# Optimization experiments

Hardware: AMD Instinct MI355X
Metric: run time of the kernel (lower is better)

The kernel has to match this reference:

```python
import jax, jax.numpy as jnp
import numpy as np

NEG_SLOPE = 0.2  # PyG GATv2Conv default negative_slope
EPS = 1e-16      # PyG softmax denominator eps


def _gatv2_conv(x, src, dst, Wl, bl, Wr, br, att, bias, heads, out_ch):
    """PyG GATv2Conv (share_weights=False, concat=True, self-loops already in edges)."""
    N = x.shape[0]
    xl = (x @ Wl + bl).reshape(N, heads, out_ch)  # values / source transform
    xr = (x @ Wr + br).reshape(N, heads, out_ch)  # target transform
    m = jax.nn.leaky_relu(xl[src] + xr[dst], NEG_SLOPE)      # [E,H,C]
    e = jnp.einsum('ehc,hc->eh', m, att)                      # [E,H]
    emax = jax.ops.segment_max(e, dst, num_segments=N)       # [N,H]
    ee = jnp.exp(e - emax[dst])
    denom = jax.ops.segment_sum(ee, dst, num_segments=N)
    alpha = ee / (denom[dst] + EPS)                           # scatter-softmax over dst
    out = jax.ops.segment_sum(xl[src] * alpha[:, :, None], dst, num_segments=N)
    return out.reshape(N, heads * out_ch) + bias


def setup_inputs() -> dict:
    key = jax.random.key(0)
    ks = jax.random.split(key, 16)
    N, E, DIN, DH, H, DOUT = 50000, 800000, 128, 16, 8, 64
    x = jax.random.normal(ks[0], (N, DIN), dtype=jnp.float32)
    edge_index = jax.random.randint(ks[1], (2, E), 0, N, dtype=jnp.int64)
    g = lambda k, shape: jax.random.normal(k, shape, dtype=jnp.float32) * (1.0 / np.sqrt(shape[0]))
    params = {
        'Wl1': g(ks[2], (DIN, H * DH)), 'bl1': jnp.zeros((H * DH,), jnp.float32),
        'Wr1': g(ks[3], (DIN, H * DH)), 'br1': jnp.zeros((H * DH,), jnp.float32),
        'att1': g(ks[4], (H, DH)), 'bias1': jnp.zeros((H * DH,), jnp.float32),
        'Wl2': g(ks[5], (H * DH, DOUT)), 'bl2': jnp.zeros((DOUT,), jnp.float32),
        'Wr2': g(ks[6], (H * DH, DOUT)), 'br2': jnp.zeros((DOUT,), jnp.float32),
        'att2': g(ks[7], (1, DOUT)), 'bias2': jnp.zeros((DOUT,), jnp.float32),
    }
    return {'x': x, 'edge_index': edge_index, **params}


def reference(x, edge_index, Wl1, bl1, Wr1, br1, att1, bias1,
              Wl2, bl2, Wr2, br2, att2, bias2):
    N = x.shape[0]
    loop = jnp.arange(N, dtype=edge_index.dtype)
    ei = jnp.concatenate([edge_index, jnp.stack([loop, loop])], axis=1)  # add self-loops
    src, dst = ei[0], ei[1]
    # eval mode: F.dropout is identity (p=0.6 dropouts skipped)
    h = _gatv2_conv(x, src, dst, Wl1, bl1, Wr1, br1, att1, bias1, heads=8, out_ch=16)
    h = jax.nn.elu(h)
    h = _gatv2_conv(h, src, dst, Wl2, bl2, Wr2, br2, att2, bias2, heads=1, out_ch=64)
    out = jax.nn.log_softmax(h, axis=1)
    predictions = jnp.argmax(out, axis=1)
    return (h, out, predictions)
```

## Files before the change

### kernel.cpp

```cpp
#include <hip/hip_runtime.h>
#include <hip/hip_bf16.h>

typedef unsigned short u16;
typedef __attribute__((ext_vector_type(8))) short bf8v;
typedef __attribute__((ext_vector_type(4))) float f4v;

#define N_NODES 50000
#define N_EDGES 800000
#define ET (N_EDGES + N_NODES)
#define D1 128
#define D2 64
#define NEG 0.2f
#define EPSF 1e-16f
#define NTILES_PAD 3128
#define NP (NTILES_PAD * 16)

#define O_XL1    0
#define O_XR1    6400000
#define O_AH     12800000
#define O_AM     16003072
#define O_AL     19206144
#define O_B1H    22409216
#define O_B1M    22425600
#define O_B1L    22441984
#define O_B2H    22458368
#define O_B2M    22466560
#define O_B2L    22474752
#define O_WF     22482944
#define O_SRC    22483968
#define O_DST    22908968
#define O_DEG    23333968
#define O_ROWPTR 23383968
#define O_RANK   23433969
#define O_CSR    23858969
#define O_FLAGS  24283969
#define O_PART   24283971

#define W_BL1   0
#define W_BR1   128
#define W_ATT1  256
#define W_BIAS1 384
#define W_BL2   512
#define W_BR2   576
#define W_ATT2  640
#define W_BIAS2 704

#define NB_SCAN  196
#define NB_CVT   3321
#define NB_PACKX 3128
#define NB_PK    (NB_SCAN + NB_PACKX + 128 + 64 + 1)
#define NB_G1    3128
#define NB_SG    (NB_G1 + NB_CVT)

__device__ __forceinline__ float load_f32(const void* src, int i, int isbf16) {
    if (isbf16) {
        u16 u = ((const u16*)src)[i];
        return __uint_as_float((unsigned)u << 16);
    }
    return ((const float*)src)[i];
}
__device__ __forceinline__ u16 f2b(float v) {
    __hip_bfloat16 h = __float2bfloat16(v);
    return *(u16*)&h;
}
__device__ __forceinline__ float b2f(u16 u) { return __uint_as_float((unsigned)u << 16); }

__device__ __forceinline__ void split3(float v, u16& hi, u16& mid, u16& lo) {
    hi = f2b(v);
    float r1 = v - b2f(hi);
    mid = f2b(r1);
    float r2 = r1 - b2f(mid);
    lo = f2b(r2);
}

__global__ void init_k(int* deg, const u16* x16, const int* ei32, int* flags) {
    int b = blockIdx.x;
    if (b < NB_SCAN) {
        int i = b * 256 + threadIdx.x;
        if (i < N_NODES) deg[i] = 0;
        return;
    }
    int lane = threadIdx.x;
    if (lane >= 64) return;
    int hits = 0;
    for (int j = lane; j < 32768; j += 64) {
        u16 u = x16[2 * j];
        if (((u >> 7) & 0xFF) == 0xFF) hits++;
    }
#pragma unroll
    for (int off = 32; off > 0; off >>= 1) hits += __shfl_xor(hits, off);
    int nz = 0;
    if (lane < 32) nz = ei32[2 * lane + 1];
#pragma unroll
    for (int off = 32; off > 0; off >>= 1) nz |= __shfl_xor(nz, off);
    if (lane == 0) { flags[0] = hits ? 0 : 1; flags[1] = nz ? 0 : 1; }
}

__global__ void cvt_k(const int* __restrict__ ei, const int* __restrict__ flags,
                      u16* __restrict__ srcA, u16* __restrict__ dstA,
                      u16* __restrict__ rank, int* __restrict__ deg) {
    int e = blockIdx.x * 256 + threadIdx.x;
    if (e >= ET) return;
    int s, d;
    if (e < N_EDGES) {
        if (flags[1]) { s = ei[2 * e]; d = ei[2 * (N_EDGES + e)]; }
        else          { s = ei[e];     d = ei[N_EDGES + e]; }
    } else {
        s = d = e - N_EDGES;
    }
    srcA[e] = (u16)s; dstA[e] = (u16)d;
    rank[e] = (u16)atomicAdd(&deg[d], 1);
}

__global__ void pk_k(const int* __restrict__ deg, int* __restrict__ part,
                     const void* x, u16* AH, u16* AM, u16* AL,
                     const void* Wl1, const void* Wr1, u16* B1H, u16* B1M, u16* B1L,
                     const void* Wl2, const void* Wr2, u16* B2H, u16* B2M, u16* B2L,
                     const void* bl1, const void* br1, const void* att1, const void* bias1,
                     const void* bl2, const void* br2, const void* att2, const void* bias2,
                     float* Wf, const int* flags) {
    int b = blockIdx.x, t = threadIdx.x;
    int fb = flags[0];
    if (b < NB_SCAN) {
        __shared__ int s[256];
        int i = b * 256 + t;
        s[t] = (i < N_NODES) ? deg[i] : 0;
        __syncthreads();
        for (int off = 128; off > 0; off >>= 1) {
            if (t < off) s[t] += s[t + off];
            __syncthreads();
        }
        if (t == 0) part[b] = s[0];
        return;
    }
    b -= NB_SCAN;
    if (b < NB_PACKX) {
        int i = b * 256 + t;
        int j = i * 8;
        int tile = j >> 11;
        int jj = j & 2047;
        int r = tile * 16 + ((jj >> 3) & 15);
        int k0 = (jj >> 7) * 8;
        uint4 H = {0, 0, 0, 0}, M = {0, 0, 0, 0}, L = {0, 0, 0, 0};
        u16* Hp = (u16*)&H; u16* Mp = (u16*)&M; u16* Lp = (u16*)&L;
        if (r < N_NODES) {
            if (fb) {
                H = *(const uint4*)((const u16*)x + r * D1 + k0);
            } else {
                float4 xa = *(const float4*)((const float*)x + r * D1 + k0);
                float4 xb = *(const float4*)((const float*)x + r * D1 + k0 + 4);
                float vv[8] = {xa.x, xa.y, xa.z, xa.w, xb.x, xb.y, xb.z, xb.w};
#pragma unroll
                for (int e2 = 0; e2 < 8; e2++) split3(vv[e2], Hp[e2], Mp[e2], Lp[e2]);
            }
        }
        *(uint4*)(AH + j) = H;
        *(uint4*)(AM + j) = M;
        *(uint4*)(AL + j) = L;
        return;
    }
    b -= NB_PACKX;
    if (b < 128) {
        int i = b * 256 + t;
        int k = i >> 8, n = i & 255;
        float v = (n < 128) ? load_f32(Wl1, k * 128 + n, fb)
                            : load_f32(Wr1, k * 128 + (n - 128), fb);
        u16 hi, mid, lo; split3(v, hi, mid, lo);
        int idx = ((k >> 3) * 256 + n) * 8 + (k & 7);
        B1H[idx] = hi; B1M[idx] = mid; B1L[idx] = lo;
        return;
    }
    b -= 128;
    if (b < 64) {
        int i = b * 256 + t;
        int k = i >> 7, n = i & 127;
        float v = (n < 64) ? load_f32(Wl2, k * 64 + n, fb)
                           : load_f32(Wr2, k * 64 + (n - 64), fb);
        u16 hi, mid, lo; split3(v, hi, mid, lo);
        int idx = ((k >> 3) * 128 + n) * 8 + (k & 7);
        B2H[idx] = hi; B2M[idx] = mid; B2L[idx] = lo;
        return;
    }
    if (t < 128) {
        Wf[W_BL1 + t]   = load_f32(bl1, t, fb);
        Wf[W_BR1 + t]   = load_f32(br1, t, fb);
        Wf[W_ATT1 + t]  = load_f32(att1, t, fb);
        Wf[W_BIAS1 + t] = load_f32(bias1, t, fb);
        if (t < 64) {
            Wf[W_BL2 + t]   = load_f32(bl2, t, fb);
            Wf[W_BR2 + t]   = load_f32(br2, t, fb);
            Wf[W_ATT2 + t]  = load_f32(att2, t, fb);
            Wf[W_BIAS2 + t] = load_f32(bias2, t, fb);
        }
    }
}

__global__ __launch_bounds__(256) void scanB_k(int* __restrict__ part) {
    __shared__ int s[256];
    int t = threadIdx.x;
    s[t] = (t < NB_SCAN) ? part[t] : 0;
    __syncthreads();
    for (int off = 1; off < 256; off <<= 1) {
        int v = (t >= off) ? s[t - off] : 0;
        __syncthreads();
        s[t] += v;
        __syncthreads();
    }
    if (t < NB_SCAN) part[t] = (t == 0) ? 0 : s[t - 1];
}

__global__ __launch_bounds__(256) void scanC_k(const int* __restrict__ deg, const int* __restrict__ part,
                                               int* __restrict__ rowptr) {
    __shared__ int s[256];
    int t = threadIdx.x, i = blockIdx.x * 256 + t;
    int v = (i < N_NODES) ? deg[i] : 0;
    s[t] = v;
    __syncthreads();
    for (int off = 1; off < 256; off <<= 1) {
        int u = (t >= off) ? s[t - off] : 0;
        __syncthreads();
        s[t] += u;
        __syncthreads();
    }
    int excl = part[blockIdx.x] + s[t] - v;
    if (i < N_NODES) rowptr[i] = excl;
    if (i == N_NODES - 1) rowptr[N_NODES] = excl + v;
}

#define MFMA6(acc, ah, am, al, bh, bm, bl)                                    \
    acc = __builtin_amdgcn_mfma_f32_16x16x32_bf16(ah, bl, acc, 0, 0, 0);      \
    acc = __builtin_amdgcn_mfma_f32_16x16x32_bf16(am, bm, acc, 0, 0, 0);      \
    acc = __builtin_amdgcn_mfma_f32_16x16x32_bf16(al, bh, acc, 0, 0, 0);      \
    acc = __builtin_amdgcn_mfma_f32_16x16x32_bf16(ah, bm, acc, 0, 0, 0);      \
    acc = __builtin_amdgcn_mfma_f32_16x16x32_bf16(am, bh, acc, 0, 0, 0);      \
    acc = __builtin_amdgcn_mfma_f32_16x16x32_bf16(ah, bh, acc, 0, 0, 0);

__global__ __launch_bounds__(256) void sg_k(const u16* __restrict__ AH, const u16* __restrict__ AM,
                                            const u16* __restrict__ AL,
                                            const u16* __restrict__ BH, const u16* __restrict__ BM,
                                            const u16* __restrict__ BL,
                                            const float* __restrict__ Wf,
                                            float* __restrict__ xl, float* __restrict__ xr,
                                            const u16* __restrict__ srcA, const u16* __restrict__ dstA,
                                            const u16* __restrict__ rank, const int* __restrict__ rowptr,
                                            u16* __restrict__ csr) {
    int b = blockIdx.x;
    if (b < NB_G1) {
        int w = threadIdx.x >> 6, l = threadIdx.x & 63;
        int tile = (b >> 2) * 4 + w;
        int cb = (b & 3) << 6;
        int lr = l & 15, lg = l >> 4;
        f4v acc[4];
#pragma unroll
        for (int nt = 0; nt < 4; nt++) acc[nt] = (f4v)(0.f);
        int aoff = tile * 2048 + lg * 128 + lr * 8;
#pragma unroll
        for (int ks = 0; ks < 4; ks++) {
            bf8v ah = *(const bf8v*)(AH + aoff + ks * 512);
            bf8v am = *(const bf8v*)(AM + aoff + ks * 512);
            bf8v al = *(const bf8v*)(AL + aoff + ks * 512);
            int boff = ((ks * 4 + lg) * 256 + cb + lr) * 8;
#pragma unroll
            for (int nt = 0; nt < 4; nt++) {
                bf8v bh = *(const bf8v*)(BH + boff + nt * 128);
                bf8v bm = *(const bf8v*)(BM + boff + nt * 128);
                bf8v bl = *(const bf8v*)(BL + boff + nt * 128);
                MFMA6(acc[nt], ah, am, al, bh, bm, bl)
            }
        }
        int r0 = tile * 16 + lg * 4;
        if (r0 >= N_NODES) return;
#pragma unroll
        for (int nt = 0; nt < 4; nt++) {
            int col = cb + nt * 16 + lr;
            float bias = (col < D1) ? Wf[W_BL1 + col] : Wf[W_BR1 + col - D1];
            float* dst = (col < D1) ? (xl + col) : (xr + col - D1);
#pragma unroll
            for (int j = 0; j < 4; j++) {
                int row = r0 + j;
                dst[(size_t)row * D1] = acc[nt][j] + bias;
            }
        }
        return;
    }
    int e = (b - NB_G1) * 256 + threadIdx.x;
    if (e < ET) {
        int d = dstA[e];
        csr[rowptr[d] + rank[e]] = srcA[e];
    }
}

__global__ __launch_bounds__(256) void gemm2_mfma(const u16* __restrict__ AH, const u16* __restrict__ AM,
                                                  const u16* __restrict__ AL,
                                                  const u16* __restrict__ BH, const u16* __restrict__ BM,
                                                  const u16* __restrict__ BL,
                                                  const float* __restrict__ Wf,
                                                  float* __restrict__ xl2, float* __restrict__ xr2) {
    int w = threadIdx.x >> 6, l = threadIdx.x & 63;
    int tile = blockIdx.x * 4 + w;
    int cb = blockIdx.y << 6;
    int lr = l & 15, lg = l >> 4;
    f4v acc[4];
#pragma unroll
    for (int nt = 0; nt < 4; nt++) acc[nt] = (f4v)(0.f);
    int aoff = tile * 2048 + lg * 128 + lr * 8;
#pragma unroll
    for (int ks = 0; ks < 4; ks++) {
        bf8v ah = *(const bf8v*)(AH + aoff + ks * 512);
        bf8v am = *(const bf8v*)(AM + aoff + ks * 512);
        bf8v al = *(const bf8v*)(AL + aoff + ks * 512);
        int boff = ((ks * 4 + lg) * 128 + cb + lr) * 8;
#pragma unroll
        for (int nt = 0; nt < 4; nt++) {
            bf8v bh = *(const bf8v*)(BH + boff + nt * 128);
            bf8v bm = *(const bf8v*)(BM + boff + nt * 128);
            bf8v bl = *(const bf8v*)(BL + boff + nt * 128);
            MFMA6(acc[nt], ah, am, al, bh, bm, bl)
        }
    }
    int r0 = tile * 16 + lg * 4;
    if (r0 >= N_NODES) return;
#pragma unroll
    for (int nt = 0; nt < 4; nt++) {
        int col = cb + nt * 16 + lr;
        float bias = (col < D2) ? Wf[W_BL2 + col] : Wf[W_BR2 + col - D2];
        float* dst = (col < D2) ? (xl2 + col) : (xr2 + col - D2);
#pragma unroll
        for (int j = 0; j < 4; j++) {
            int row = r0 + j;
            dst[(size_t)row * D2] = acc[nt][j] + bias;
        }
    }
}

#define L1STEP(a)                                                              \
    {                                                                          \
        float m0 = a.x + xr4.x; m0 = fmaxf(m0, NEG * m0);                      \
        float m1 = a.y + xr4.y; m1 = fmaxf(m1, NEG * m1);                      \
        float m2 = a.z + xr4.z; m2 = fmaxf(m2, NEG * m2);                      \
        float m3 = a.w + xr4.w; m3 = fmaxf(m3, NEG * m3);                      \
        float p = m0 * at4.x + m1 * at4.y + m2 * at4.z + m3 * at4.w;           \
        p += __shfl_xor(p, 1);                                                 \
        p += __shfl_xor(p, 2);                                                 \
        p = fminf(fmaxf(p, -60.f), 60.f);                                      \
        float wgt = __expf(p);                                                 \
        l += wgt;                                                              \
        acc.x = fmaf(wgt, a.x, acc.x);                                         \
        acc.y = fmaf(wgt, a.y, acc.y);                                         \
        acc.z = fmaf(wgt, a.z, acc.z);                                         \
        acc.w = fmaf(wgt, a.w, acc.w);                                         \
    }

__global__ __launch_bounds__(256) void l1_agg(const int* __restrict__ rowptr, const u16* __restrict__ csr,
                                              const float* __restrict__ xl, const float* __restrict__ xr,
                                              const float* __restrict__ Wf,
                                              u16* __restrict__ A2H, u16* __restrict__ A2M, u16* __restrict__ A2L) {
    int n = (blockIdx.x * 256 + threadIdx.x) >> 5;
    int q = threadIdx.x & 31;
    const float4* xl4 = (const float4*)xl;
    float4 xr4 = ((const float4*)(xr + (size_t)n * D1))[q];
    float4 at4 = ((const float4*)(Wf + W_ATT1))[q];
    int i0 = rowptr[n], i1 = rowptr[n + 1];
    float l = 0.f;
    float4 acc = {0.f, 0.f, 0.f, 0.f};
    float4 a = xl4[(size_t)csr[i0] * 32 + q];
    for (int i = i0 + 1; i < i1; i++) {
        float4 an = xl4[(size_t)csr[i] * 32 + q];
        L1STEP(a)
        a = an;
    }
    L1STEP(a)
    float rinv = 1.f / l;
    float4 bi4 = ((const float4*)(Wf + W_BIAS1))[q];
    float v0 = acc.x * rinv + bi4.x; v0 = v0 > 0.f ? v0 : expm1f(v0);
    float v1 = acc.y * rinv + bi4.y; v1 = v1 > 0.f ? v1 : expm1f(v1);
    float v2 = acc.z * rinv + bi4.z; v2 = v2 > 0.f ? v2 : expm1f(v2);
    float v3 = acc.w * rinv + bi4.w; v3 = v3 > 0.f ? v3 : expm1f(v3);
    int base = (n >> 4) * 2048 + (q >> 1) * 128 + (n & 15) * 8 + (q & 1) * 4;
    ushort4 h4, m4, l4;
    split3(v0, h4.x, m4.x, l4.x);
    split3(v1, h4.y, m4.y, l4.y);
    split3(v2, h4.z, m4.z, l4.z);
    split3(v3, h4.w, m4.w, l4.w);
    *(ushort4*)(A2H + base) = h4;
    *(ushort4*)(A2M + base) = m4;
    *(ushort4*)(A2L + base) = l4;
}

#define L2STEP(a)                                                              \
    {                                                                          \
        float m0 = a.x + xr4.x; m0 = fmaxf(m0, NEG * m0);                      \
        float m1 = a.y + xr4.y; m1 = fmaxf(m1, NEG * m1);                      \
        float m2 = a.z + xr4.z; m2 = fmaxf(m2, NEG * m2);                      \
        float m3 = a.w + xr4.w; m3 = fmaxf(m3, NEG * m3);                      \
        float p = m0 * at4.x + m1 * at4.y + m2 * at4.z + m3 * at4.w;           \
        p += __shfl_xor(p, 1);                                                 \
        p += __shfl_xor(p, 2);                                                 \
        p += __shfl_xor(p, 4);                                                 \
        p += __shfl_xor(p, 8);                                                 \
        p = fminf(fmaxf(p, -80.f), 80.f);                                      \
        float wgt = __expf(p);                                                 \
        l += wgt;                                                              \
        acc.x = fmaf(wgt, a.x, acc.x);                                         \
        acc.y = fmaf(wgt, a.y, acc.y);                                         \
        acc.z = fmaf(wgt, a.z, acc.z);                                         \
        acc.w = fmaf(wgt, a.w, acc.w);                                         \
    }

__global__ __launch_bounds__(256) void l2_agg(const int* __restrict__ rowptr, const u16* __restrict__ csr,
                                              const float* __restrict__ xl, const float* __restrict__ xr,
                                              const float* __restrict__ Wf, float* __restrict__ out) {
    int n = (blockIdx.x * 256 + threadIdx.x) >> 4;
    int q = threadIdx.x & 15;
    const float4* xl4 = (const float4*)xl;
    float4 xr4 = ((const float4*)(xr + (size_t)n * D2))[q];
    float4 at4 = ((const float4*)(Wf + W_ATT2))[q];
    int i0 = rowptr[n], i1 = rowptr[n + 1];
    float l = 0.f;
    float4 acc = {0.f, 0.f, 0.f, 0.f};
    float4 a = xl4[(size_t)csr[i0] * 16 + q];
    for (int i = i0 + 1; i < i1; i++) {
        float4 an = xl4[(size_t)csr[i] * 16 + q];
        L2STEP(a)
        a = an;
    }
    L2STEP(a)
    float rinv = 1.f / (l + EPSF);
    float4 bi4 = ((const float4*)(Wf + W_BIAS2))[q];
    float v0 = acc.x * rinv + bi4.x;
    float v1 = acc.y * rinv + bi4.y;
    float v2 = acc.z * rinv + bi4.z;
    float v3 = acc.w * rinv + bi4.w;
    float4 hv = {v0, v1, v2, v3};
    ((float4*)(out + (size_t)n * D2))[q] = hv;
    float mx = fmaxf(fmaxf(v0, v1), fmaxf(v2, v3));
#pragma unroll
    for (int off = 1; off < 16; off <<= 1) mx = fmaxf(mx, __shfl_xor(mx, off));
    float sum = expf(v0 - mx) + expf(v1 - mx) + expf(v2 - mx) + expf(v3 - mx);
#pragma unroll
    for (int off = 1; off < 16; off <<= 1) sum += __shfl_xor(sum, off);
    float lse = mx + logf(sum);
    float4 ls = {v0 - lse, v1 - lse, v2 - lse, v3 - lse};
    ((float4*)(out + (size_t)N_NODES * D2 + (size_t)n * D2))[q] = ls;
    float bv = v0; int bi = 4 * q;
    if (v1 > bv) { bv = v1; bi = 4 * q + 1; }
    if (v2 > bv) { bv = v2; bi = 4 * q + 2; }
    if (v3 > bv) { bv = v3; bi = 4 * q + 3; }
#pragma unroll
    for (int off = 1; off < 16; off <<= 1) {
        float ov = __shfl_xor(bv, off);
        int   oi = __shfl_xor(bi, off);
        if (ov > bv || (ov == bv && oi < bi)) { bv = ov; bi = oi; }
    }
    if (q == 0) out[(size_t)2 * N_NODES * D2 + n] = (float)bi;
}

extern "C" void kernel_launch(void* const* d_in, const int* in_sizes, int n_in,
                              void* d_out, int out_size, void* d_ws, size_t ws_size,
                              hipStream_t stream) {
    const void* x  = d_in[0];
    const int*  ei = (const int*)d_in[1];

    float* ws = (float*)d_ws;
    float* xl1    = ws + O_XL1;
    float* xr1    = ws + O_XR1;
    u16*   AH     = (u16*)(ws + O_AH);
    u16*   AM     = (u16*)(ws + O_AM);
    u16*   AL     = (u16*)(ws + O_AL);
    u16*   B1H    = (u16*)(ws + O_B1H);
    u16*   B1M    = (u16*)(ws + O_B1M);
    u16*   B1L    = (u16*)(ws + O_B1L);
    u16*   B2H    = (u16*)(ws + O_B2H);
    u16*   B2M    = (u16*)(ws + O_B2M);
    u16*   B2L    = (u16*)(ws + O_B2L);
    float* Wf     = ws + O_WF;
    u16*   srcA   = (u16*)(ws + O_SRC);
    u16*   dstA   = (u16*)(ws + O_DST);
    int*   deg    = (int*)(ws + O_DEG);
    int*   rowptr = (int*)(ws + O_ROWPTR);
    u16*   rank   = (u16*)(ws + O_RANK);
    u16*   csr    = (u16*)(ws + O_CSR);
    int*   flags  = (int*)(ws + O_FLAGS);
    int*   part   = (int*)(ws + O_PART);

    float* xl2 = xl1;
    float* xr2 = xl1 + 3200000;

    init_k<<<NB_SCAN + 1, 256, 0, stream>>>(deg, (const u16*)x, ei, flags);
    cvt_k<<<NB_CVT, 256, 0, stream>>>(ei, flags, srcA, dstA, rank, deg);
    pk_k<<<NB_PK, 256, 0, stream>>>(deg, part,
                                    x, AH, AM, AL,
                                    d_in[2], d_in[4], B1H, B1M, B1L,
                                    d_in[8], d_in[10], B2H, B2M, B2L,
                                    d_in[3], d_in[5], d_in[6], d_in[7],
                                    d_in[9], d_in[11], d_in[12], d_in[13],
                                    Wf, flags);
    scanB_k<<<1, 256, 0, stream>>>(part);
    scanC_k<<<NB_SCAN, 256, 0, stream>>>(deg, part, rowptr);
    sg_k<<<NB_SG, 256, 0, stream>>>(AH, AM, AL, B1H, B1M, B1L, Wf, xl1, xr1,
                                    srcA, dstA, rank, rowptr, csr);

    l1_agg<<<6250, 256, 0, stream>>>(rowptr, csr, xl1, xr1, Wf, AH, AM, AL);
    gemm2_mfma<<<dim3(NTILES_PAD / 4, 2), 256, 0, stream>>>(AH, AM, AL, B2H, B2M, B2L, Wf, xl2, xr2);
    l2_agg<<<3125, 256, 0, stream>>>(rowptr, csr, xl2, xr2, Wf, (float*)d_out);
}
```

Before: 254.9 us.

## Degree-sort nodes for aggregation load balance and fuse prep kernels

Builds a degree histogram and counting-sort permutation of nodes, so each aggregation warp group in layer 1 and layer 2 handles nodes of similar degree and divergence within a wave is reduced. The edge-convert kernel is merged into the packing kernel, which removes one launch. Layer-1 output is now written as plain fp32 and split into three bf16 parts inside gemm2, replacing the tiled hi/mid/lo writes. The cost is three extra small scan/histogram passes, atomics on the bucket cursors, and redundant split work in gemm2 because each of its two column blocks reads the same rows.

```diff
diff --git a/kernel.cpp b/kernel.cpp
--- a/kernel.cpp
+++ b/kernel.cpp
@@ -35,6 +35,9 @@
 #define O_CSR    23858969
 #define O_FLAGS  24283969
 #define O_PART   24283971
+#define O_HIST   24284167
+#define O_BCUR   24284423
+#define O_PERM   24284679
 
 #define W_BL1   0
 #define W_BR1   128
@@ -48,7 +51,7 @@
 #define NB_SCAN  196
 #define NB_CVT   3321
 #define NB_PACKX 3128
-#define NB_PK    (NB_SCAN + NB_PACKX + 128 + 64 + 1)
+#define NB_PREP  (NB_CVT + NB_PACKX + 128 + 64 + 1)
 #define NB_G1    3128
 #define NB_SG    (NB_G1 + NB_CVT)
 
@@ -73,11 +76,15 @@
     lo = f2b(r2);
 }
 
-__global__ void init_k(int* deg, const u16* x16, const int* ei32, int* flags) {
+__global__ void init_k(int* deg, const u16* x16, const int* ei32, int* flags, int* hist) {
     int b = blockIdx.x;
     if (b < NB_SCAN) {
         int i = b * 256 + threadIdx.x;
         if (i < N_NODES) deg[i] = 0;
+        return;
+    }
+    if (b == NB_SCAN + 1) {
+        hist[threadIdx.x] = 0;
         return;
     }
     int lane = threadIdx.x;
@@ -96,44 +103,33 @@
     if (lane == 0) { flags[0] = hits ? 0 : 1; flags[1] = nz ? 0 : 1; }
 }
 
-__global__ void cvt_k(const int* __restrict__ ei, const int* __restrict__ flags,
-                      u16* __restrict__ srcA, u16* __restrict__ dstA,
-                      u16* __restrict__ rank, int* __restrict__ deg) {
-    int e = blockIdx.x * 256 + threadIdx.x;
-    if (e >= ET) return;
-    int s, d;
-    if (e < N_EDGES) {
-        if (flags[1]) { s = ei[2 * e]; d = ei[2 * (N_EDGES + e)]; }
-        else          { s = ei[e];     d = ei[N_EDGES + e]; }
-    } else {
-        s = d = e - N_EDGES;
-    }
-    srcA[e] = (u16)s; dstA[e] = (u16)d;
-    rank[e] = (u16)atomicAdd(&deg[d], 1);
-}
-
-__global__ void pk_k(const int* __restrict__ deg, int* __restrict__ part,
-                     const void* x, u16* AH, u16* AM, u16* AL,
-                     const void* Wl1, const void* Wr1, u16* B1H, u16* B1M, u16* B1L,
-                     const void* Wl2, const void* Wr2, u16* B2H, u16* B2M, u16* B2L,
-                     const void* bl1, const void* br1, const void* att1, const void* bias1,
-                     const void* bl2, const void* br2, const void* att2, const void* bias2,
-                     float* Wf, const int* flags) {
+__global__ void prep_k(const int* __restrict__ ei,
+                       u16* __restrict__ srcA, u16* __restrict__ dstA,
+                       u16* __restrict__ rank, int* __restrict__ deg,
+                       const void* x, u16* AH, u16* AM, u16* AL,
+                       const void* Wl1, const void* Wr1, u16* B1H, u16* B1M, u16* B1L,
+                       const void* Wl2, const void* Wr2, u16* B2H, u16* B2M, u16* B2L,
+                       const void* bl1, const void* br1, const void* att1, const void* bias1,
+                       const void* bl2, const void* br2, const void* att2, const void* bias2,
+                       float* Wf, const int* flags) {
     int b = blockIdx.x, t = threadIdx.x;
     int fb = flags[0];
-    if (b < NB_SCAN) {
-        __shared__ int s[256];
-        int i = b * 256 + t;
-        s[t] = (i < N_NODES) ? deg[i] : 0;
-        __syncthreads();
-        for (int off = 128; off > 0; off >>= 1) {
-            if (t < off) s[t] += s[t + off];
-            __syncthreads();
-        }
-        if (t == 0) part[b] = s[0];
-        return;
-    }
-    b -= NB_SCAN;
+    if (b < NB_CVT) {
+        int e = b * 256 + t;
+        if (e < ET) {
+            int s, d;
+            if (e < N_EDGES) {
+                if (flags[1]) { s = ei[2 * e]; d = ei[2 * (N_EDGES + e)]; }
+                else          { s = ei[e];     d = ei[N_EDGES + e]; }
+            } else {
+                s = d = e - N_EDGES;
+            }
+            srcA[e] = (u16)s; dstA[e] = (u16)d;
+            rank[e] = (u16)atomicAdd(&deg[d], 1);
+        }
+        return;
+    }
+    b -= NB_CVT;
     if (b < NB_PACKX) {
         int i = b * 256 + t;
         int j = i * 8;
@@ -195,10 +191,43 @@
     }
 }
 
-__global__ __launch_bounds__(256) void scanB_k(int* __restrict__ part) {
+__global__ __launch_bounds__(256) void sa_k(const int* __restrict__ deg, int* __restrict__ part,
+                                            int* __restrict__ hist) {
+    int b = blockIdx.x, t = threadIdx.x;
+    if (b < NB_SCAN) {
+        __shared__ int s[256];
+        int i = b * 256 + t;
+        s[t] = (i < N_NODES) ? deg[i] : 0;
+        __syncthreads();
+        for (int off = 128; off > 0; off >>= 1) {
+            if (t < off) s[t] += s[t + off];
+            __syncthreads();
+        }
+        if (t == 0) part[b] = s[0];
+        return;
+    }
+    int i = (b - NB_SCAN) * 256 + t;
+    if (i < N_NODES) atomicAdd(&hist[min(deg[i], 255)], 1);
+}
+
+__global__ __launch_bounds__(256) void sb_k(int* __restrict__ part, const int* __restrict__ hist,
+                                            int* __restrict__ bcur) {
     __shared__ int s[256];
     int t = threadIdx.x;
-    s[t] = (t < NB_SCAN) ? part[t] : 0;
+    if (blockIdx.x == 0) {
+        s[t] = (t < NB_SCAN) ? part[t] : 0;
+        __syncthreads();
+        for (int off = 1; off < 256; off <<= 1) {
+            int v = (t >= off) ? s[t - off] : 0;
+            __syncthreads();
+            s[t] += v;
+            __syncthreads();
+        }
+        if (t < NB_SCAN) part[t] = (t == 0) ? 0 : s[t - 1];
+        return;
+    }
+    int h = hist[t];
+    s[t] = h;
     __syncthreads();
     for (int off = 1; off < 256; off <<= 1) {
         int v = (t >= off) ? s[t - off] : 0;
@@ -206,25 +235,35 @@
         s[t] += v;
         __syncthreads();
     }
-    if (t < NB_SCAN) part[t] = (t == 0) ? 0 : s[t - 1];
-}
-
-__global__ __launch_bounds__(256) void scanC_k(const int* __restrict__ deg, const int* __restrict__ part,
-                                               int* __restrict__ rowptr) {
-    __shared__ int s[256];
-    int t = threadIdx.x, i = blockIdx.x * 256 + t;
-    int v = (i < N_NODES) ? deg[i] : 0;
-    s[t] = v;
-    __syncthreads();
-    for (int off = 1; off < 256; off <<= 1) {
-        int u = (t >= off) ? s[t - off] : 0;
+    bcur[t] = s[t] - h;
+}
+
+__global__ __launch_bounds__(256) void sc_k(const int* __restrict__ deg, const int* __restrict__ part,
+                                            int* __restrict__ rowptr,
+                                            int* __restrict__ bcur, int* __restrict__ perm) {
+    int b = blockIdx.x, t = threadIdx.x;
+    if (b < NB_SCAN) {
+        __shared__ int s[256];
+        int i = b * 256 + t;
+        int v = (i < N_NODES) ? deg[i] : 0;
+        s[t] = v;
         __syncthreads();
-        s[t] += u;
-        __syncthreads();
-    }
-    int excl = part[blockIdx.x] + s[t] - v;
-    if (i < N_NODES) rowptr[i] = excl;
-    if (i == N_NODES - 1) rowptr[N_NODES] = excl + v;
+        for (int off = 1; off < 256; off <<= 1) {
+            int u = (t >= off) ? s[t - off] : 0;
+            __syncthreads();
+            s[t] += u;
+            __syncthreads();
+        }
+        int excl = part[b] + s[t] - v;
+        if (i < N_NODES) rowptr[i] = excl;
+        if (i == N_NODES - 1) rowptr[N_NODES] = excl + v;
+        return;
+    }
+    int i = (b - NB_SCAN) * 256 + t;
+    if (i < N_NODES) {
+        int bk = min(deg[i], 255);
+        perm[atomicAdd(&bcur[bk], 1)] = i;
+    }
 }
 
 #define MFMA6(acc, ah, am, al, bh, bm, bl)                                    \
@@ -290,8 +329,8 @@
     }
 }
 
-__global__ __launch_bounds__(256) void gemm2_mfma(const u16* __restrict__ AH, const u16* __restrict__ AM,
-                                                  const u16* __restrict__ AL,
+union bfu { bf8v v; u16 s[8]; };
+__global__ __launch_bounds__(256) void gemm2_mfma(const float* __restrict__ hA,
                                                   const u16* __restrict__ BH, const u16* __restrict__ BM,
                                                   const u16* __restrict__ BL,
                                                   const float* __restrict__ Wf,
@@ -300,22 +339,27 @@
     int tile = blockIdx.x * 4 + w;
     int cb = blockIdx.y << 6;
     int lr = l & 15, lg = l >> 4;
+    int r = tile * 16 + lr;
+    int rc = min(r, N_NODES - 1);
     f4v acc[4];
 #pragma unroll
     for (int nt = 0; nt < 4; nt++) acc[nt] = (f4v)(0.f);
-    int aoff = tile * 2048 + lg * 128 + lr * 8;
 #pragma unroll
     for (int ks = 0; ks < 4; ks++) {
-        bf8v ah = *(const bf8v*)(AH + aoff + ks * 512);
-        bf8v am = *(const bf8v*)(AM + aoff + ks * 512);
-        bf8v al = *(const bf8v*)(AL + aoff + ks * 512);
+        const float* hp = hA + (size_t)rc * D1 + ks * 32 + lg * 8;
+        float4 p0 = *(const float4*)hp;
+        float4 p1 = *(const float4*)(hp + 4);
+        float vv[8] = {p0.x, p0.y, p0.z, p0.w, p1.x, p1.y, p1.z, p1.w};
+        bfu ah, am, al;
+#pragma unroll
+        for (int j = 0; j < 8; j++) split3(vv[j], ah.s[j], am.s[j], al.s[j]);
         int boff = ((ks * 4 + lg) * 128 + cb + lr) * 8;
 #pragma unroll
         for (int nt = 0; nt < 4; nt++) {
             bf8v bh = *(const bf8v*)(BH + boff + nt * 128);
             bf8v bm = *(const bf8v*)(BM + boff + nt * 128);
             bf8v bl = *(const bf8v*)(BL + boff + nt * 128);
-            MFMA6(acc[nt], ah, am, al, bh, bm, bl)
+            MFMA6(acc[nt], ah.v, am.v, al.v, bh, bm, bl)
         }
     }
     int r0 = tile * 16 + lg * 4;
@@ -352,10 +396,10 @@
     }
 
 __global__ __launch_bounds__(256) void l1_agg(const int* __restrict__ rowptr, const u16* __restrict__ csr,
+                                              const int* __restrict__ perm,
                                               const float* __restrict__ xl, const float* __restrict__ xr,
-                                              const float* __restrict__ Wf,
-                                              u16* __restrict__ A2H, u16* __restrict__ A2M, u16* __restrict__ A2L) {
-    int n = (blockIdx.x * 256 + threadIdx.x) >> 5;
+                                              const float* __restrict__ Wf, float* __restrict__ hbuf) {
+    int n = perm[(blockIdx.x * 256 + threadIdx.x) >> 5];
     int q = threadIdx.x & 31;
     const float4* xl4 = (const float4*)xl;
     float4 xr4 = ((const float4*)(xr + (size_t)n * D1))[q];
@@ -376,15 +420,8 @@
     float v1 = acc.y * rinv + bi4.y; v1 = v1 > 0.f ? v1 : expm1f(v1);
     float v2 = acc.z * rinv + bi4.z; v2 = v2 > 0.f ? v2 : expm1f(v2);
     float v3 = acc.w * rinv + bi4.w; v3 = v3 > 0.f ? v3 : expm1f(v3);
-    int base = (n >> 4) * 2048 + (q >> 1) * 128 + (n & 15) * 8 + (q & 1) * 4;
-    ushort4 h4, m4, l4;
-    split3(v0, h4.x, m4.x, l4.x);
-    split3(v1, h4.y, m4.y, l4.y);
-    split3(v2, h4.z, m4.z, l4.z);
-    split3(v3, h4.w, m4.w, l4.w);
-    *(ushort4*)(A2H + base) = h4;
-    *(ushort4*)(A2M + base) = m4;
-    *(ushort4*)(A2L + base) = l4;
+    float4 hv = {v0, v1, v2, v3};
+    ((float4*)(hbuf + (size_t)n * D1))[q] = hv;
 }
 
 #define L2STEP(a)                                                              \
@@ -408,9 +445,10 @@
     }
 
 __global__ __launch_bounds__(256) void l2_agg(const int* __restrict__ rowptr, const u16* __restrict__ csr,
+                                              const int* __restrict__ perm,
                                               const float* __restrict__ xl, const float* __restrict__ xr,
                                               const float* __restrict__ Wf, float* __restrict__ out) {
-    int n = (blockIdx.x * 256 + threadIdx.x) >> 4;
+    int n = perm[(blockIdx.x * 256 + threadIdx.x) >> 4];
     int q = threadIdx.x & 15;
     const float4* xl4 = (const float4*)xl;
     float4 xr4 = ((const float4*)(xr + (size_t)n * D2))[q];
@@ -467,6 +505,7 @@
     u16*   AH     = (u16*)(ws + O_AH);
     u16*   AM     = (u16*)(ws + O_AM);
     u16*   AL     = (u16*)(ws + O_AL);
+    float* hbuf   = ws + O_AH;
     u16*   B1H    = (u16*)(ws + O_B1H);
     u16*   B1M    = (u16*)(ws + O_B1M);
     u16*   B1L    = (u16*)(ws + O_B1L);
@@ -482,25 +521,28 @@
     u16*   csr    = (u16*)(ws + O_CSR);
     int*   flags  = (int*)(ws + O_FLAGS);
     int*   part   = (int*)(ws + O_PART);
+    int*   hist   = (int*)(ws + O_HIST);
+    int*   bcur   = (int*)(ws + O_BCUR);
+    int*   perm   = (int*)(ws + O_PERM);
 
     float* xl2 = xl1;
     float* xr2 = xl1 + 3200000;
 
-    init_k<<<NB_SCAN + 1, 256, 0, stream>>>(deg, (const u16*)x, ei, flags);
-    cvt_k<<<NB_CVT, 256, 0, stream>>>(ei, flags, srcA, dstA, rank, deg);
-    pk_k<<<NB_PK, 256, 0, stream>>>(deg, part,
-                                    x, AH, AM, AL,
-                                    d_in[2], d_in[4], B1H, B1M, B1L,
-                                    d_in[8], d_in[10], B2H, B2M, B2L,
-                                    d_in[3], d_in[5], d_in[6], d_in[7],
-                                    d_in[9], d_in[11], d_in[12], d_in[13],
-                                    Wf, flags);
-    scanB_k<<<1, 256, 0, stream>>>(part);
-    scanC_k<<<NB_SCAN, 256, 0, stream>>>(deg, part, rowptr);
+    init_k<<<NB_SCAN + 2, 256, 0, stream>>>(deg, (const u16*)x, ei, flags, hist);
+    prep_k<<<NB_PREP, 256, 0, stream>>>(ei, srcA, dstA, rank, deg,
+                                        x, AH, AM, AL,
+                                        d_in[2], d_in[4], B1H, B1M, B1L,
+                                        d_in[8], d_in[10], B2H, B2M, B2L,
+                                        d_in[3], d_in[5], d_in[6], d_in[7],
+                                        d_in[9], d_in[11], d_in[12], d_in[13],
+                                        Wf, flags);
+    sa_k<<<2 * NB_SCAN, 256, 0, stream>>>(deg, part, hist);
+    sb_k<<<2, 256, 0, stream>>>(part, hist, bcur);
+    sc_k<<<2 * NB_SCAN, 256, 0, stream>>>(deg, part, rowptr, bcur, perm);
     sg_k<<<NB_SG, 256, 0, stream>>>(AH, AM, AL, B1H, B1M, B1L, Wf, xl1, xr1,
                                     srcA, dstA, rank, rowptr, csr);
 
-    l1_agg<<<6250, 256, 0, stream>>>(rowptr, csr, xl1, xr1, Wf, AH, AM, AL);
-    gemm2_mfma<<<dim3(NTILES_PAD / 4, 2), 256, 0, stream>>>(AH, AM, AL, B2H, B2M, B2L, Wf, xl2, xr2);
-    l2_agg<<<3125, 256, 0, stream>>>(rowptr, csr, xl2, xr2, Wf, (float*)d_out);
-}
+    l1_agg<<<6250, 256, 0, stream>>>(rowptr, csr, perm, xl1, xr1, Wf, hbuf);
+    gemm2_mfma<<<dim3(NTILES_PAD / 4, 2), 256, 0, stream>>>(hbuf, B2H, B2M, B2L, Wf, xl2, xr2);
+    l2_agg<<<3125, 256, 0, stream>>>(rowptr, csr, perm, xl2, xr2, Wf, (float*)d_out);
+}
```

Result: slower. 541.9 us (+112.5%).
